# Optimization experiments

Hardware: AMD Instinct MI355X
Metric: run time of the kernel (lower is better)

Reference implementation:

```python
import jax, jax.numpy as jnp
import numpy as np

B, D, L, H = 512, 512, 32, 300  # batch, input_dim, latent_dim, hidden_dim


def setup_inputs() -> dict:
    key = jax.random.key(0)
    ks = jax.random.split(key, 16)
    s = lambda k, *sh: jax.random.normal(k, sh, dtype=jnp.float32) * 0.05
    return {
        "x": jax.random.normal(ks[0], (B, D), dtype=jnp.float32),
        "eps": jax.random.normal(ks[1], (B, L), dtype=jnp.float32),
        "W": jax.random.normal(ks[2], (D, L), dtype=jnp.float32),  # mask (get_generator_mask -> W)
        "qz_w1": s(ks[3], D, H), "qz_b1": s(ks[4], H),
        "qz_w2": s(ks[5], H, H), "qz_b2": s(ks[6], H),
        "zm_w": s(ks[7], H, L), "zm_b": s(ks[8], L),
        "zl_w": s(ks[9], H, L), "zl_b": s(ks[10], L),
        "gen_w1": s(ks[11], L, H),               # no bias (bias=False)
        "gen_w2": s(ks[12], H, H), "gen_b2": s(ks[13], H),
        "col_w": s(ks[14], D, H), "col_b": s(ks[15], D),  # stacked column_means Linears
    }


def reference(x, eps, W, qz_w1, qz_b1, qz_w2, qz_b2, zm_w, zm_b, zl_w, zl_b,
              gen_w1, gen_w2, gen_b2, col_w, col_b):
    # encode
    h = jax.nn.relu(x @ qz_w1 + qz_b1)
    h = jax.nn.relu(h @ qz_w2 + qz_b2)
    z_mean = h @ zm_w + zm_b
    z_log_var = h @ zl_w + zl_b
    # reparameterize (eps supplied as input)
    z = z_mean + eps * jnp.exp(0.5 * z_log_var)
    # decode: per-column masked generator MLP, batched over columns j
    masked = W[:, None, :] * z[None, :, :]                 # [D, B, L]
    g = jax.nn.relu(jnp.einsum('jbl,lh->jbh', masked, gen_w1))
    g = jax.nn.relu(jnp.einsum('jbh,hk->jbk', g, gen_w2) + gen_b2)
    x_rec = jnp.einsum('jbh,jh->jb', g, col_w) + col_b[:, None]  # [D, B]
    x_mean = x_rec.T                                       # [B, D]
    return (x_mean, z, z_mean, z_log_var)
```

## Files before the change

kernel.cpp:

```cpp
#include <hip/hip_runtime.h>

#define B_ 512
#define D_ 512
#define L_ 32
#define H_ 300
#define HP 304
#define NT 19
#define NS 10
#define G1S 312
#define KSPLIT 0

typedef unsigned short ushort_t;
typedef __bf16 bf16x8 __attribute__((ext_vector_type(8)));
typedef float f32x4 __attribute__((ext_vector_type(4)));

__device__ __forceinline__ ushort_t f2bf(float f) {
    unsigned int u = __float_as_uint(f);
    u += 0x7fffu + ((u >> 16) & 1u);
    return (ushort_t)(u >> 16);
}
__device__ __forceinline__ int kbase0(int grp) { return KSPLIT ? 4 * grp : 8 * grp; }
__device__ __forceinline__ int kbase1(int grp) { return KSPLIT ? 16 + 4 * grp : 8 * grp + 4; }

template<int K, int N>
__global__ __launch_bounds__(256) void mlp_relu_kernel(const float* __restrict__ in,
        const float* __restrict__ w, const float* __restrict__ bias,
        float* __restrict__ out) {
    __shared__ float rs[K];
    int row = blockIdx.x;
    for (int k = threadIdx.x; k < K; k += 256) rs[k] = in[row * K + k];
    __syncthreads();
    for (int c = threadIdx.x; c < N; c += 256) {
        float acc = bias[c];
        #pragma unroll 4
        for (int k = 0; k < K; ++k) acc = fmaf(rs[k], w[k * N + c], acc);
        out[row * N + c] = fmaxf(acc, 0.f);
    }
}

__global__ __launch_bounds__(64) void latent_kernel(const float* __restrict__ h2,
        const float* __restrict__ eps,
        const float* __restrict__ zm_w, const float* __restrict__ zm_b,
        const float* __restrict__ zl_w, const float* __restrict__ zl_b,
        float* __restrict__ out, float* __restrict__ ws_z) {
    __shared__ float hs[H_];
    __shared__ float zm_s[L_], zl_s[L_];
    int row = blockIdx.x;
    int t = threadIdx.x;
    for (int k = t; k < H_; k += 64) hs[k] = h2[row * H_ + k];
    __syncthreads();
    {
        int l = t & 31;
        const float* wp = (t < 32) ? zm_w : zl_w;
        const float* bp = (t < 32) ? zm_b : zl_b;
        float acc = bp[l];
        #pragma unroll 4
        for (int k = 0; k < H_; ++k) acc = fmaf(hs[k], wp[k * L_ + l], acc);
        if (t < 32) zm_s[l] = acc; else zl_s[l] = acc;
    }
    __syncthreads();
    if (t < 32) {
        float zm = zm_s[t], zl = zl_s[t];
        float zv = zm + eps[row * L_ + t] * expf(0.5f * zl);
        float* z_out  = out + B_ * D_;
        float* zm_out = out + B_ * D_ + B_ * L_;
        float* zl_out = out + B_ * D_ + 2 * B_ * L_;
        z_out[row * L_ + t]  = zv;
        zm_out[row * L_ + t] = zm;
        zl_out[row * L_ + t] = zl;
        ws_z[row * L_ + t]   = zv;
    }
}

__global__ __launch_bounds__(64) void prep_kernel(const float* __restrict__ gw1,
        const float* __restrict__ gw2, ushort_t* __restrict__ gw1f,
        ushort_t* __restrict__ gw2f) {
    int blk = blockIdx.x;
    int l = threadIdx.x;
    int grp = l >> 4, li = l & 15;
    union { ushort_t u[8]; uint4 q; } V;
    if (blk < NT) {
        int nt = blk;
        int n = nt * 16 + li;
        #pragma unroll
        for (int i = 0; i < 8; ++i) {
            int k = (i < 4) ? kbase0(grp) + i : kbase1(grp) + (i - 4);
            V.u[i] = f2bf((n < H_) ? gw1[k * H_ + n] : 0.f);
        }
        *reinterpret_cast<uint4*>(gw1f + (nt * 64 + l) * 8) = V.q;
    } else {
        int idx = blk - NT;
        int nt = idx / NS, s = idx % NS;
        int n = nt * 16 + li;
        #pragma unroll
        for (int i = 0; i < 8; ++i) {
            int k = 32 * s + ((i < 4) ? kbase0(grp) + i : kbase1(grp) + (i - 4));
            V.u[i] = f2bf((k < H_ && n < H_) ? gw2[k * H_ + n] : 0.f);
        }
        *reinterpret_cast<uint4*>(gw2f + ((nt * NS + s) * 64 + l) * 8) = V.q;
    }
}

__global__ __launch_bounds__(256, 3) void decode_kernel(
        const float* __restrict__ z, const float* __restrict__ Wmask,
        const ushort_t* __restrict__ gw1f, const ushort_t* __restrict__ gw2f,
        const float* __restrict__ gb2, const float* __restrict__ colw,
        const float* __restrict__ colb, float* __restrict__ xmean) {
    __shared__ __align__(16) ushort_t mf[4 * 64 * 8];
    __shared__ __align__(16) ushort_t g1s[64 * G1S + 16];
    __shared__ float xrec[64];

    const int j    = blockIdx.y;
    const int b0   = blockIdx.x * 64;
    const int tid  = threadIdx.x;
    const int w    = tid >> 6;
    const int lane = tid & 63;
    const int grp  = lane >> 4, li = lane & 15;

    {
        int b = b0 + w * 16 + li;
        union { ushort_t u[8]; uint4 q; } V;
        #pragma unroll
        for (int i = 0; i < 8; ++i) {
            int k = (i < 4) ? kbase0(grp) + i : kbase1(grp) + (i - 4);
            V.u[i] = f2bf(Wmask[j * L_ + k] * z[b * L_ + k]);
        }
        *reinterpret_cast<uint4*>(&mf[(w * 64 + lane) * 8]) = V.q;
        if (tid < 64) xrec[tid] = 0.f;
        for (int idx = tid; idx < 64 * 8 + 16; idx += 256) {
            int r = idx >> 3, c = HP + (idx & 7);
            g1s[(idx < 512) ? (r * G1S + c) : (64 * G1S + (idx - 512))] = 0;
        }
    }
    __syncthreads();

    const int nlocal = (w == 3) ? 4 : 5;

    {
        bf16x8 am[4];
        #pragma unroll
        for (int mt = 0; mt < 4; ++mt)
            am[mt] = *reinterpret_cast<const bf16x8*>(&mf[(mt * 64 + lane) * 8]);
        #pragma unroll
        for (int ntl = 0; ntl < 5; ++ntl) {
            if (ntl < nlocal) {
                int nt = w * 5 + ntl;
                bf16x8 bfr = *reinterpret_cast<const bf16x8*>(gw1f + (nt * 64 + lane) * 8);
                int h = nt * 16 + li;
                #pragma unroll
                for (int mt = 0; mt < 4; ++mt) {
                    f32x4 c = {0.f, 0.f, 0.f, 0.f};
                    c = __builtin_amdgcn_mfma_f32_16x16x32_bf16(am[mt], bfr, c, 0, 0, 0);
                    #pragma unroll
                    for (int r = 0; r < 4; ++r) {
                        int m = mt * 16 + grp * 4 + r;
                        g1s[m * G1S + h] = f2bf(fmaxf(c[r], 0.f));
                    }
                }
            }
        }
    }
    __syncthreads();

    {
        f32x4 acc[4][5];
        #pragma unroll
        for (int mt = 0; mt < 4; ++mt)
            #pragma unroll
            for (int n = 0; n < 5; ++n) acc[mt][n] = {0.f, 0.f, 0.f, 0.f};

        for (int s = 0; s < NS; ++s) {
            bf16x8 af[4];
            #pragma unroll
            for (int mt = 0; mt < 4; ++mt) {
                const ushort_t* p = &g1s[(mt * 16 + li) * G1S + 32 * s];
                union { bf16x8 v; uint2 d[2]; } U;
                U.d[0] = *reinterpret_cast<const uint2*>(p + kbase0(grp));
                U.d[1] = *reinterpret_cast<const uint2*>(p + kbase1(grp));
                af[mt] = U.v;
            }
            #pragma unroll
            for (int ntl = 0; ntl < 5; ++ntl) {
                if (ntl < nlocal) {
                    int nt = w * 5 + ntl;
                    bf16x8 bfr = *reinterpret_cast<const bf16x8*>(
                        gw2f + ((nt * NS + s) * 64 + lane) * 8);
                    #pragma unroll
                    for (int mt = 0; mt < 4; ++mt)
                        acc[mt][ntl] = __builtin_amdgcn_mfma_f32_16x16x32_bf16(
                            af[mt], bfr, acc[mt][ntl], 0, 0, 0);
                }
            }
        }

        float partial[4][4] = {};
        #pragma unroll
        for (int ntl = 0; ntl < 5; ++ntl) {
            if (ntl < nlocal) {
                int h = (w * 5 + ntl) * 16 + li;
                float bias = 0.f, fac = 0.f;
                if (h < H_) { bias = gb2[h]; fac = colw[j * H_ + h]; }
                #pragma unroll
                for (int mt = 0; mt < 4; ++mt)
                    #pragma unroll
                    for (int r = 0; r < 4; ++r)
                        partial[mt][r] += fmaxf(acc[mt][ntl][r] + bias, 0.f) * fac;
            }
        }
        #pragma unroll
        for (int mt = 0; mt < 4; ++mt)
            #pragma unroll
            for (int r = 0; r < 4; ++r) {
                float v = partial[mt][r];
                v += __shfl_xor(v, 1);
                v += __shfl_xor(v, 2);
                v += __shfl_xor(v, 4);
                v += __shfl_xor(v, 8);
                if (li == 0) atomicAdd(&xrec[mt * 16 + grp * 4 + r], v);
            }
    }
    __syncthreads();

    if (tid < 64) xmean[(size_t)(b0 + tid) * D_ + j] = xrec[tid] + colb[j];
}

extern "C" void kernel_launch(void* const* d_in, const int* in_sizes, int n_in,
                              void* d_out, int out_size, void* d_ws, size_t ws_size,
                              hipStream_t stream) {
    const float* x     = (const float*)d_in[0];
    const float* eps   = (const float*)d_in[1];
    const float* Wm    = (const float*)d_in[2];
    const float* qz_w1 = (const float*)d_in[3];
    const float* qz_b1 = (const float*)d_in[4];
    const float* qz_w2 = (const float*)d_in[5];
    const float* qz_b2 = (const float*)d_in[6];
    const float* zm_w  = (const float*)d_in[7];
    const float* zm_b  = (const float*)d_in[8];
    const float* zl_w  = (const float*)d_in[9];
    const float* zl_b  = (const float*)d_in[10];
    const float* gw1   = (const float*)d_in[11];
    const float* gw2   = (const float*)d_in[12];
    const float* gb2   = (const float*)d_in[13];
    const float* colw  = (const float*)d_in[14];
    const float* colb  = (const float*)d_in[15];
    float* out = (float*)d_out;
    float* ws  = (float*)d_ws;

    float* h1 = ws;
    float* h2 = ws + 153600;
    float* zb = ws + 307200;
    ushort_t* gw1f = (ushort_t*)ws;
    ushort_t* gw2f = (ushort_t*)ws + 19 * 64 * 8;

    mlp_relu_kernel<512, 300><<<512, 256, 0, stream>>>(x,  qz_w1, qz_b1, h1);
    mlp_relu_kernel<300, 300><<<512, 256, 0, stream>>>(h1, qz_w2, qz_b2, h2);
    latent_kernel<<<512, 64, 0, stream>>>(h2, eps, zm_w, zm_b, zl_w, zl_b, out, zb);
    prep_kernel<<<NT + NT * NS, 64, 0, stream>>>(gw1, gw2, gw1f, gw2f);
    decode_kernel<<<dim3(8, 512), 256, 0, stream>>>(zb, Wm, gw1f, gw2f, gb2, colw, colb, out);
}
```

Baseline: 137.1 us.

## Move encoder layers to split-bf16 MFMA GEMMs and pipeline decode weight loads

The scalar per-row FP32 encoder kernels and the latent kernel are replaced by MFMA GEMMs. These split both activations and weights into bf16 hi/lo parts and use three MFMA passes to keep near-FP32 accuracy. The prep kernel now also packs the encoder weights, and the z_mean/z_log_var projection is fused with the reparameterization. In the decode kernel, the k-ordering is simplified so fragments load as single 16-byte vectors, and the mask/z inputs are loaded as float4. The first-layer MFMA operands are swapped so ReLU results are stored packed, and the gw2 fragments for the next k-step are prefetched. The encoder grids are small (32 blocks), which limits parallelism, and the 3-pass bf16 split adds MFMA work and a small accuracy risk.

```diff
diff --git a/kernel.cpp b/kernel.cpp
--- a/kernel.cpp
+++ b/kernel.cpp
@@ -4,100 +4,193 @@
 #define D_ 512
 #define L_ 32
 #define H_ 300
-#define HP 304
 #define NT 19
 #define NS 10
 #define G1S 312
-#define KSPLIT 0
 
 typedef unsigned short ushort_t;
 typedef __bf16 bf16x8 __attribute__((ext_vector_type(8)));
 typedef float f32x4 __attribute__((ext_vector_type(4)));
 
+__device__ __forceinline__ float bf2f(unsigned int hi16) {
+    return __uint_as_float(hi16 << 16);
+}
 __device__ __forceinline__ ushort_t f2bf(float f) {
     unsigned int u = __float_as_uint(f);
     u += 0x7fffu + ((u >> 16) & 1u);
     return (ushort_t)(u >> 16);
 }
-__device__ __forceinline__ int kbase0(int grp) { return KSPLIT ? 4 * grp : 8 * grp; }
-__device__ __forceinline__ int kbase1(int grp) { return KSPLIT ? 16 + 4 * grp : 8 * grp + 4; }
-
-template<int K, int N>
-__global__ __launch_bounds__(256) void mlp_relu_kernel(const float* __restrict__ in,
-        const float* __restrict__ w, const float* __restrict__ bias,
-        float* __restrict__ out) {
-    __shared__ float rs[K];
-    int row = blockIdx.x;
-    for (int k = threadIdx.x; k < K; k += 256) rs[k] = in[row * K + k];
+__device__ __forceinline__ unsigned int pack2(float a, float b) {
+    return (unsigned int)f2bf(a) | ((unsigned int)f2bf(b) << 16);
+}
+
+union B8 { ushort_t u[8]; uint4 q; bf16x8 v; };
+
+__global__ __launch_bounds__(64) void prep_kernel(
+        const float* __restrict__ gw1, const float* __restrict__ gw2,
+        const float* __restrict__ qw1, const float* __restrict__ qw2,
+        const float* __restrict__ zmw, const float* __restrict__ zlw,
+        ushort_t* __restrict__ gw1f, ushort_t* __restrict__ gw2f,
+        ushort_t* __restrict__ w1hi, ushort_t* __restrict__ w1lo,
+        ushort_t* __restrict__ w2hi, ushort_t* __restrict__ w2lo,
+        ushort_t* __restrict__ w3hi, ushort_t* __restrict__ w3lo) {
+    int blk = blockIdx.x;
+    int l = threadIdx.x, grp = l >> 4, li = l & 15;
+    if (blk < 209) {
+        const float* src; int K, nt, s; ushort_t* dst;
+        if (blk < 19) { nt = blk; s = 0; src = gw1; K = 32; dst = gw1f + (nt * 64 + l) * 8; }
+        else { int i = blk - 19; nt = i / 10; s = i % 10; src = gw2; K = 300;
+               dst = gw2f + ((nt * 10 + s) * 64 + l) * 8; }
+        int n = nt * 16 + li;
+        B8 V;
+        #pragma unroll
+        for (int i = 0; i < 8; ++i) {
+            int k = 32 * s + 8 * grp + i;
+            V.u[i] = f2bf((k < K && n < H_) ? src[k * H_ + n] : 0.f);
+        }
+        *reinterpret_cast<uint4*>(dst) = V.q;
+    } else {
+        const float* src = nullptr; int K, N, nt, s, stacked = 0;
+        ushort_t *dh, *dl;
+        if (blk < 513)      { int i = blk - 209; nt = i / 16; s = i % 16; src = qw1; K = 512; N = 300;
+                              dh = w1hi + ((nt * 16 + s) * 64 + l) * 8; dl = w1lo + ((nt * 16 + s) * 64 + l) * 8; }
+        else if (blk < 703) { int i = blk - 513; nt = i / 10; s = i % 10; src = qw2; K = 300; N = 300;
+                              dh = w2hi + ((nt * 10 + s) * 64 + l) * 8; dl = w2lo + ((nt * 10 + s) * 64 + l) * 8; }
+        else                { int i = blk - 703; nt = i / 10; s = i % 10; K = 300; N = 64; stacked = 1;
+                              dh = w3hi + ((nt * 10 + s) * 64 + l) * 8; dl = w3lo + ((nt * 10 + s) * 64 + l) * 8; }
+        int n = nt * 16 + li;
+        B8 Vh, Vl;
+        #pragma unroll
+        for (int i = 0; i < 8; ++i) {
+            int k = 32 * s + 8 * grp + i;
+            float v = 0.f;
+            if (k < K && n < N) {
+                if (!stacked) v = src[k * N + n];
+                else          v = (n < 32) ? zmw[k * 32 + n] : zlw[k * 32 + (n - 32)];
+            }
+            ushort_t h = f2bf(v);
+            Vh.u[i] = h;
+            Vl.u[i] = f2bf(v - bf2f(h));
+        }
+        *reinterpret_cast<uint4*>(dh) = Vh.q;
+        *reinterpret_cast<uint4*>(dl) = Vl.q;
+    }
+}
+
+template<int KSTEPS, int NTILES, bool RELU>
+__global__ __launch_bounds__(256) void enc_gemm_f32(const float* __restrict__ A, int lda,
+        const ushort_t* __restrict__ Whi, const ushort_t* __restrict__ Wlo,
+        const float* __restrict__ bias, float* __restrict__ out, int ldo, int Ncols) {
+    const int tid = threadIdx.x;
+    const int w = tid >> 6, lane = tid & 63;
+    const int grp = lane >> 4, li = lane & 15;
+    const int r0 = blockIdx.x * 16;
+    constexpr int NTL = (NTILES + 3) / 4;
+    const int nbeg = w * NTL;
+    int nl = NTILES - nbeg; if (nl < 0) nl = 0; if (nl > NTL) nl = NTL;
+    const int nlocal = nl;
+
+    f32x4 acc[NTL];
+    #pragma unroll
+    for (int i = 0; i < NTL; ++i) acc[i] = {0.f, 0.f, 0.f, 0.f};
+
+    for (int s = 0; s < KSTEPS; ++s) {
+        int kb = 32 * s + 8 * grp;
+        B8 Ah, Al;
+        if (kb < lda) {
+            const float* ap = A + (size_t)(r0 + li) * lda + kb;
+            float4 f0 = *reinterpret_cast<const float4*>(ap);
+            float4 f1 = *reinterpret_cast<const float4*>(ap + 4);
+            float fv[8] = {f0.x, f0.y, f0.z, f0.w, f1.x, f1.y, f1.z, f1.w};
+            #pragma unroll
+            for (int i = 0; i < 8; ++i) {
+                ushort_t h = f2bf(fv[i]);
+                Ah.u[i] = h;
+                Al.u[i] = f2bf(fv[i] - bf2f(h));
+            }
+        } else {
+            Ah.q = make_uint4(0, 0, 0, 0);
+            Al.q = make_uint4(0, 0, 0, 0);
+        }
+        #pragma unroll
+        for (int ntl = 0; ntl < NTL; ++ntl) {
+            if (ntl < nlocal) {
+                int nt = nbeg + ntl;
+                bf16x8 bh = *reinterpret_cast<const bf16x8*>(
+                    Whi + ((size_t)(nt * KSTEPS + s) * 64 + lane) * 8);
+                bf16x8 bl = *reinterpret_cast<const bf16x8*>(
+                    Wlo + ((size_t)(nt * KSTEPS + s) * 64 + lane) * 8);
+                acc[ntl] = __builtin_amdgcn_mfma_f32_16x16x32_bf16(Ah.v, bh, acc[ntl], 0, 0, 0);
+                acc[ntl] = __builtin_amdgcn_mfma_f32_16x16x32_bf16(Al.v, bh, acc[ntl], 0, 0, 0);
+                acc[ntl] = __builtin_amdgcn_mfma_f32_16x16x32_bf16(Ah.v, bl, acc[ntl], 0, 0, 0);
+            }
+        }
+    }
+    #pragma unroll
+    for (int ntl = 0; ntl < NTL; ++ntl) {
+        if (ntl < nlocal) {
+            int h = (nbeg + ntl) * 16 + li;
+            float bv = (bias != nullptr && h < Ncols) ? bias[h] : 0.f;
+            #pragma unroll
+            for (int r = 0; r < 4; ++r) {
+                float v = acc[ntl][r] + bv;
+                if (RELU) v = fmaxf(v, 0.f);
+                if (h >= Ncols) v = 0.f;
+                out[(size_t)(r0 + 4 * grp + r) * ldo + h] = v;
+            }
+        }
+    }
+}
+
+__global__ __launch_bounds__(256) void enc3_reparam(const float* __restrict__ h2,
+        const ushort_t* __restrict__ w3hi, const ushort_t* __restrict__ w3lo,
+        const float* __restrict__ zmb, const float* __restrict__ zlb,
+        const float* __restrict__ eps, float* __restrict__ out, float* __restrict__ zb) {
+    __shared__ float zs[16][64];
+    const int tid = threadIdx.x;
+    const int w = tid >> 6, lane = tid & 63;
+    const int grp = lane >> 4, li = lane & 15;
+    const int r0 = blockIdx.x * 16;
+
+    f32x4 acc = {0.f, 0.f, 0.f, 0.f};
+    for (int s = 0; s < 10; ++s) {
+        int kb = 32 * s + 8 * grp;
+        B8 Ah, Al;
+        if (kb < 304) {
+            const float* ap = h2 + (size_t)(r0 + li) * 304 + kb;
+            float4 f0 = *reinterpret_cast<const float4*>(ap);
+            float4 f1 = *reinterpret_cast<const float4*>(ap + 4);
+            float fv[8] = {f0.x, f0.y, f0.z, f0.w, f1.x, f1.y, f1.z, f1.w};
+            #pragma unroll
+            for (int i = 0; i < 8; ++i) {
+                ushort_t h = f2bf(fv[i]);
+                Ah.u[i] = h;
+                Al.u[i] = f2bf(fv[i] - bf2f(h));
+            }
+        } else {
+            Ah.q = make_uint4(0, 0, 0, 0);
+            Al.q = make_uint4(0, 0, 0, 0);
+        }
+        bf16x8 bh = *reinterpret_cast<const bf16x8*>(w3hi + ((size_t)(w * 10 + s) * 64 + lane) * 8);
+        bf16x8 bl = *reinterpret_cast<const bf16x8*>(w3lo + ((size_t)(w * 10 + s) * 64 + lane) * 8);
+        acc = __builtin_amdgcn_mfma_f32_16x16x32_bf16(Ah.v, bh, acc, 0, 0, 0);
+        acc = __builtin_amdgcn_mfma_f32_16x16x32_bf16(Al.v, bh, acc, 0, 0, 0);
+        acc = __builtin_amdgcn_mfma_f32_16x16x32_bf16(Ah.v, bl, acc, 0, 0, 0);
+    }
+    #pragma unroll
+    for (int r = 0; r < 4; ++r) zs[4 * grp + r][w * 16 + li] = acc[r];
     __syncthreads();
-    for (int c = threadIdx.x; c < N; c += 256) {
-        float acc = bias[c];
-        #pragma unroll 4
-        for (int k = 0; k < K; ++k) acc = fmaf(rs[k], w[k * N + c], acc);
-        out[row * N + c] = fmaxf(acc, 0.f);
-    }
-}
-
-__global__ __launch_bounds__(64) void latent_kernel(const float* __restrict__ h2,
-        const float* __restrict__ eps,
-        const float* __restrict__ zm_w, const float* __restrict__ zm_b,
-        const float* __restrict__ zl_w, const float* __restrict__ zl_b,
-        float* __restrict__ out, float* __restrict__ ws_z) {
-    __shared__ float hs[H_];
-    __shared__ float zm_s[L_], zl_s[L_];
-    int row = blockIdx.x;
-    int t = threadIdx.x;
-    for (int k = t; k < H_; k += 64) hs[k] = h2[row * H_ + k];
-    __syncthreads();
-    {
-        int l = t & 31;
-        const float* wp = (t < 32) ? zm_w : zl_w;
-        const float* bp = (t < 32) ? zm_b : zl_b;
-        float acc = bp[l];
-        #pragma unroll 4
-        for (int k = 0; k < H_; ++k) acc = fmaf(hs[k], wp[k * L_ + l], acc);
-        if (t < 32) zm_s[l] = acc; else zl_s[l] = acc;
-    }
-    __syncthreads();
-    if (t < 32) {
-        float zm = zm_s[t], zl = zl_s[t];
-        float zv = zm + eps[row * L_ + t] * expf(0.5f * zl);
-        float* z_out  = out + B_ * D_;
-        float* zm_out = out + B_ * D_ + B_ * L_;
-        float* zl_out = out + B_ * D_ + 2 * B_ * L_;
-        z_out[row * L_ + t]  = zv;
-        zm_out[row * L_ + t] = zm;
-        zl_out[row * L_ + t] = zl;
-        ws_z[row * L_ + t]   = zv;
-    }
-}
-
-__global__ __launch_bounds__(64) void prep_kernel(const float* __restrict__ gw1,
-        const float* __restrict__ gw2, ushort_t* __restrict__ gw1f,
-        ushort_t* __restrict__ gw2f) {
-    int blk = blockIdx.x;
-    int l = threadIdx.x;
-    int grp = l >> 4, li = l & 15;
-    union { ushort_t u[8]; uint4 q; } V;
-    if (blk < NT) {
-        int nt = blk;
-        int n = nt * 16 + li;
-        #pragma unroll
-        for (int i = 0; i < 8; ++i) {
-            int k = (i < 4) ? kbase0(grp) + i : kbase1(grp) + (i - 4);
-            V.u[i] = f2bf((n < H_) ? gw1[k * H_ + n] : 0.f);
-        }
-        *reinterpret_cast<uint4*>(gw1f + (nt * 64 + l) * 8) = V.q;
-    } else {
-        int idx = blk - NT;
-        int nt = idx / NS, s = idx % NS;
-        int n = nt * 16 + li;
-        #pragma unroll
-        for (int i = 0; i < 8; ++i) {
-            int k = 32 * s + ((i < 4) ? kbase0(grp) + i : kbase1(grp) + (i - 4));
-            V.u[i] = f2bf((k < H_ && n < H_) ? gw2[k * H_ + n] : 0.f);
-        }
-        *reinterpret_cast<uint4*>(gw2f + ((nt * NS + s) * 64 + l) * 8) = V.q;
+
+    for (int idx = tid; idx < 512; idx += 256) {
+        int m = idx >> 5, l2 = idx & 31;
+        int row = r0 + m;
+        float zm = zs[m][l2] + zmb[l2];
+        float zl = zs[m][32 + l2] + zlb[l2];
+        float zv = zm + eps[row * 32 + l2] * expf(0.5f * zl);
+        out[B_ * D_ + row * 32 + l2] = zv;
+        out[B_ * D_ + B_ * L_ + row * 32 + l2] = zm;
+        out[B_ * D_ + 2 * B_ * L_ + row * 32 + l2] = zl;
+        zb[row * 32 + l2] = zv;
     }
 }
 
@@ -119,16 +212,21 @@
 
     {
         int b = b0 + w * 16 + li;
-        union { ushort_t u[8]; uint4 q; } V;
-        #pragma unroll
-        for (int i = 0; i < 8; ++i) {
-            int k = (i < 4) ? kbase0(grp) + i : kbase1(grp) + (i - 4);
-            V.u[i] = f2bf(Wmask[j * L_ + k] * z[b * L_ + k]);
-        }
+        const float* zp = z + (size_t)b * L_ + 8 * grp;
+        const float* wp = Wmask + (size_t)j * L_ + 8 * grp;
+        float4 z0 = *reinterpret_cast<const float4*>(zp);
+        float4 z1 = *reinterpret_cast<const float4*>(zp + 4);
+        float4 w0 = *reinterpret_cast<const float4*>(wp);
+        float4 w1 = *reinterpret_cast<const float4*>(wp + 4);
+        B8 V;
+        V.u[0] = f2bf(w0.x * z0.x); V.u[1] = f2bf(w0.y * z0.y);
+        V.u[2] = f2bf(w0.z * z0.z); V.u[3] = f2bf(w0.w * z0.w);
+        V.u[4] = f2bf(w1.x * z1.x); V.u[5] = f2bf(w1.y * z1.y);
+        V.u[6] = f2bf(w1.z * z1.z); V.u[7] = f2bf(w1.w * z1.w);
         *reinterpret_cast<uint4*>(&mf[(w * 64 + lane) * 8]) = V.q;
         if (tid < 64) xrec[tid] = 0.f;
         for (int idx = tid; idx < 64 * 8 + 16; idx += 256) {
-            int r = idx >> 3, c = HP + (idx & 7);
+            int r = idx >> 3, c = 304 + (idx & 7);
             g1s[(idx < 512) ? (r * G1S + c) : (64 * G1S + (idx - 512))] = 0;
         }
     }
@@ -137,25 +235,23 @@
     const int nlocal = (w == 3) ? 4 : 5;
 
     {
-        bf16x8 am[4];
+        bf16x8 bm[4];
         #pragma unroll
         for (int mt = 0; mt < 4; ++mt)
-            am[mt] = *reinterpret_cast<const bf16x8*>(&mf[(mt * 64 + lane) * 8]);
+            bm[mt] = *reinterpret_cast<const bf16x8*>(&mf[(mt * 64 + lane) * 8]);
         #pragma unroll
         for (int ntl = 0; ntl < 5; ++ntl) {
             if (ntl < nlocal) {
                 int nt = w * 5 + ntl;
-                bf16x8 bfr = *reinterpret_cast<const bf16x8*>(gw1f + (nt * 64 + lane) * 8);
-                int h = nt * 16 + li;
+                bf16x8 ga = *reinterpret_cast<const bf16x8*>(gw1f + (nt * 64 + lane) * 8);
                 #pragma unroll
                 for (int mt = 0; mt < 4; ++mt) {
                     f32x4 c = {0.f, 0.f, 0.f, 0.f};
-                    c = __builtin_amdgcn_mfma_f32_16x16x32_bf16(am[mt], bfr, c, 0, 0, 0);
-                    #pragma unroll
-                    for (int r = 0; r < 4; ++r) {
-                        int m = mt * 16 + grp * 4 + r;
-                        g1s[m * G1S + h] = f2bf(fmaxf(c[r], 0.f));
-                    }
+                    c = __builtin_amdgcn_mfma_f32_16x16x32_bf16(ga, bm[mt], c, 0, 0, 0);
+                    uint2 p;
+                    p.x = pack2(fmaxf(c[0], 0.f), fmaxf(c[1], 0.f));
+                    p.y = pack2(fmaxf(c[2], 0.f), fmaxf(c[3], 0.f));
+                    *reinterpret_cast<uint2*>(&g1s[(mt * 16 + li) * G1S + nt * 16 + 4 * grp]) = p;
                 }
             }
         }
@@ -169,28 +265,37 @@
             #pragma unroll
             for (int n = 0; n < 5; ++n) acc[mt][n] = {0.f, 0.f, 0.f, 0.f};
 
+        bf16x8 bcur[5], bnext[5];
+        #pragma unroll
+        for (int ntl = 0; ntl < 5; ++ntl)
+            if (ntl < nlocal)
+                bcur[ntl] = *reinterpret_cast<const bf16x8*>(
+                    gw2f + ((size_t)((w * 5 + ntl) * NS) * 64 + lane) * 8);
+
         for (int s = 0; s < NS; ++s) {
             bf16x8 af[4];
             #pragma unroll
-            for (int mt = 0; mt < 4; ++mt) {
-                const ushort_t* p = &g1s[(mt * 16 + li) * G1S + 32 * s];
-                union { bf16x8 v; uint2 d[2]; } U;
-                U.d[0] = *reinterpret_cast<const uint2*>(p + kbase0(grp));
-                U.d[1] = *reinterpret_cast<const uint2*>(p + kbase1(grp));
-                af[mt] = U.v;
+            for (int mt = 0; mt < 4; ++mt)
+                af[mt] = *reinterpret_cast<const bf16x8*>(
+                    &g1s[(mt * 16 + li) * G1S + 32 * s + 8 * grp]);
+            if (s + 1 < NS) {
+                #pragma unroll
+                for (int ntl = 0; ntl < 5; ++ntl)
+                    if (ntl < nlocal)
+                        bnext[ntl] = *reinterpret_cast<const bf16x8*>(
+                            gw2f + ((size_t)((w * 5 + ntl) * NS + s + 1) * 64 + lane) * 8);
             }
             #pragma unroll
             for (int ntl = 0; ntl < 5; ++ntl) {
                 if (ntl < nlocal) {
-                    int nt = w * 5 + ntl;
-                    bf16x8 bfr = *reinterpret_cast<const bf16x8*>(
-                        gw2f + ((nt * NS + s) * 64 + lane) * 8);
                     #pragma unroll
                     for (int mt = 0; mt < 4; ++mt)
                         acc[mt][ntl] = __builtin_amdgcn_mfma_f32_16x16x32_bf16(
-                            af[mt], bfr, acc[mt][ntl], 0, 0, 0);
+                            af[mt], bcur[ntl], acc[mt][ntl], 0, 0, 0);
                 }
             }
+            #pragma unroll
+            for (int ntl = 0; ntl < 5; ++ntl) bcur[ntl] = bnext[ntl];
         }
 
         float partial[4][4] = {};
@@ -244,17 +349,24 @@
     const float* colw  = (const float*)d_in[14];
     const float* colb  = (const float*)d_in[15];
     float* out = (float*)d_out;
-    float* ws  = (float*)d_ws;
-
-    float* h1 = ws;
-    float* h2 = ws + 153600;
-    float* zb = ws + 307200;
-    ushort_t* gw1f = (ushort_t*)ws;
-    ushort_t* gw2f = (ushort_t*)ws + 19 * 64 * 8;
-
-    mlp_relu_kernel<512, 300><<<512, 256, 0, stream>>>(x,  qz_w1, qz_b1, h1);
-    mlp_relu_kernel<300, 300><<<512, 256, 0, stream>>>(h1, qz_w2, qz_b2, h2);
-    latent_kernel<<<512, 64, 0, stream>>>(h2, eps, zm_w, zm_b, zl_w, zl_b, out, zb);
-    prep_kernel<<<NT + NT * NS, 64, 0, stream>>>(gw1, gw2, gw1f, gw2f);
+    char* ws = (char*)d_ws;
+
+    ushort_t* gw1f = (ushort_t*)(ws + 0);
+    ushort_t* gw2f = (ushort_t*)(ws + 19456);
+    ushort_t* w1hi = (ushort_t*)(ws + 214016);
+    ushort_t* w1lo = (ushort_t*)(ws + 525312);
+    ushort_t* w2hi = (ushort_t*)(ws + 836608);
+    ushort_t* w2lo = (ushort_t*)(ws + 1031168);
+    ushort_t* w3hi = (ushort_t*)(ws + 1225728);
+    ushort_t* w3lo = (ushort_t*)(ws + 1266688);
+    float*    h1   = (float*)(ws + 1307648);
+    float*    h2   = (float*)(ws + 214016);
+    float*    zb   = (float*)(ws + 1930240);
+
+    prep_kernel<<<743, 64, 0, stream>>>(gw1, gw2, qz_w1, qz_w2, zm_w, zl_w,
+                                        gw1f, gw2f, w1hi, w1lo, w2hi, w2lo, w3hi, w3lo);
+    enc_gemm_f32<16, NT, true><<<32, 256, 0, stream>>>(x, 512, w1hi, w1lo, qz_b1, h1, 304, 300);
+    enc_gemm_f32<10, NT, true><<<32, 256, 0, stream>>>(h1, 304, w2hi, w2lo, qz_b2, h2, 304, 300);
+    enc3_reparam<<<32, 256, 0, stream>>>(h2, w3hi, w3lo, zm_b, zl_b, eps, out, zb);
     decode_kernel<<<dim3(8, 512), 256, 0, stream>>>(zb, Wm, gw1f, gw2f, gb2, colw, colb, out);
 }
```

New measurement: 265.3 us. 93.5% more time.
